# Optimization experiments

Hardware: AMD Instinct MI355X
Metric: run time of the kernel (lower is better)

The kernel has to match this reference:

```python
import jax, jax.numpy as jnp
import numpy as np
import math

NUM_HEADS = 16
ATTN_WIDTH = 256


def setup_inputs() -> dict:
    key = jax.random.key(0)
    ks = jax.random.split(key, 5)
    B, S, C, H = 2, 2048, 1024, 1024
    scale = 0.02
    return {
        "x": jax.random.normal(ks[0], (B, S, C), dtype=jnp.float32),
        "Wq": jax.random.normal(ks[1], (C, H), dtype=jnp.float32) * scale,
        "Wk": jax.random.normal(ks[2], (C, H), dtype=jnp.float32) * scale,
        "Wv": jax.random.normal(ks[3], (C, H), dtype=jnp.float32) * scale,
        "Wo": jax.random.normal(ks[4], (H, C), dtype=jnp.float32) * scale,
    }


def reference(x, Wq, Wk, Wv, Wo):
    B, S, C = x.shape
    H = NUM_HEADS
    dh = Wq.shape[1] // H  # head dim; Q.size(-1) in torch code

    def split_heads(t):
        # [B, S, H*dh] -> [B, H, S, dh]
        return t.reshape(B, S, H, dh).transpose(0, 2, 1, 3)

    q = split_heads(x @ Wq)
    k = split_heads(x @ Wk)
    v = split_heads(x @ Wv)

    scores = jnp.einsum("bhqd,bhkd->bhqk", q, k) / math.sqrt(dh)
    # exp-shift (first 'softmax-like' step, unnormalized)
    scores = jnp.exp(scores - jnp.max(scores, axis=-1, keepdims=True))
    # banded mask: tril(attn_width//2 - 1).triu(-(attn_width//2))
    i = jnp.arange(S)[:, None]
    j = jnp.arange(S)[None, :]
    d = j - i
    half = ATTN_WIDTH // 2
    mask = (d <= half - 1) & (d >= -half)
    scores = jnp.where(mask, scores, 0.0)
    # second softmax over the masked exp-scores (zeros contribute exp(0)=1)
    weights = jax.nn.softmax(scores, axis=-1)

    out = jnp.einsum("bhqk,bhkd->bhqd", weights, v)  # [B, H, S, dh]
    out = out.transpose(0, 2, 1, 3).reshape(B, S, H * dh)
    return out @ Wo
```

## Files before the change

### kernel.cpp

```cpp
#include <hip/hip_runtime.h>
#include <math.h>

typedef __bf16 bf16_t;
typedef bf16_t bf16x8 __attribute__((ext_vector_type(8)));
typedef bf16_t bf16x4 __attribute__((ext_vector_type(4)));
typedef float f32x4 __attribute__((ext_vector_type(4)));

constexpr int S_ = 2048;
constexpr float SCALE = 0.125f;

#define MFMA_B16(a, b, c) __builtin_amdgcn_mfma_f32_16x16x32_bf16(a, b, c, 0, 0, 0)

#define WAIT_VM0() __builtin_amdgcn_s_waitcnt(0x0F70)
#define WAIT_VM4() __builtin_amdgcn_s_waitcnt(0x0F74)
#define BARRIER()  __builtin_amdgcn_s_barrier()

typedef __attribute__((address_space(1))) const void* as1_cvp;
typedef __attribute__((address_space(3))) void* as3_vp;

__device__ __forceinline__ void gl2lds16(const void* g, void* l)
{
    __builtin_amdgcn_global_load_lds((as1_cvp)g, (as3_vp)l, 16, 0, 0);
}

#define SRC_SWZ8(lane) ((((lane) & 3) ^ (((lane) >> 3) & 3)) * 8)
#define RD_SWZ8(quad, l15) ((((quad) ^ (((l15) >> 1) & 3))) * 8)

__global__ __launch_bounds__(256) void prep(const float* __restrict__ x,
                                            const float* __restrict__ Wq,
                                            const float* __restrict__ Wk,
                                            const float* __restrict__ Wv,
                                            const float* __restrict__ Wo,
                                            bf16_t* __restrict__ xb,
                                            bf16_t* __restrict__ Wqt,
                                            bf16_t* __restrict__ Wkt,
                                            bf16_t* __restrict__ Wvt,
                                            bf16_t* __restrict__ Wot,
                                            float* __restrict__ vsp)
{
    __shared__ float T[64][65];
    const int blk = blockIdx.x;
    const int tid = threadIdx.x;
    if (blk < 1024) {
#pragma unroll
        for (int u = 0; u < 4; ++u) {
            const int g = blk * 1024 + u * 256 + tid;
            const float4 v = ((const float4*)x)[g];
            bf16x4 o;
            o[0] = (bf16_t)v.x; o[1] = (bf16_t)v.y;
            o[2] = (bf16_t)v.z; o[3] = (bf16_t)v.w;
            *(bf16x4*)&xb[(size_t)g * 4] = o;
        }
    } else if (blk < 2048) {
        const int rem = blk - 1024;
        const int wsel = rem >> 8, t = rem & 255;
        const float* src = (wsel == 0) ? Wq : (wsel == 1) ? Wk : (wsel == 2) ? Wv : Wo;
        bf16_t* dst = (wsel == 0) ? Wqt : (wsel == 1) ? Wkt : (wsel == 2) ? Wvt : Wot;
        const int k0 = (t >> 4) * 64, n0 = (t & 15) * 64;
        const int rr = tid >> 4, c4 = (tid & 15) * 4;
#pragma unroll
        for (int u = 0; u < 4; ++u) {
            const float4 v = *(const float4*)&src[(size_t)(k0 + u * 16 + rr) * 1024 + n0 + c4];
            T[u * 16 + rr][c4 + 0] = v.x; T[u * 16 + rr][c4 + 1] = v.y;
            T[u * 16 + rr][c4 + 2] = v.z; T[u * 16 + rr][c4 + 3] = v.w;
        }
        __syncthreads();
#pragma unroll
        for (int u = 0; u < 4; ++u) {
            bf16x4 o;
#pragma unroll
            for (int e = 0; e < 4; ++e) o[e] = (bf16_t)T[c4 + e][u * 16 + rr];
            *(bf16x4*)&dst[(size_t)(n0 + u * 16 + rr) * 1024 + k0 + c4] = o;
        }
    } else {
#pragma unroll
        for (int u = 0; u < 8; ++u) vsp[u * 256 + tid] = 0.f;
    }
}

template <int MODE>
__device__ __forceinline__ void mfma_gemm_body(const bf16_t* __restrict__ A,
                                               const bf16_t* __restrict__ Bt,
                                               void* __restrict__ dst,
                                               float* __restrict__ vsum_out,
                                               int m0, int n0)
{
    __shared__ bf16_t As[12288];
    __shared__ bf16_t Bs[12288];

    const int tid = threadIdx.x;
    const int lane = tid & 63, wid = tid >> 6;
    const int l15 = lane & 15, quad = lane >> 4;
    const int wm = (wid & 1) * 64, wn = (wid >> 1) * 64;

    const int srow = wid * 32 + (lane >> 2);
    const int scg8 = SRC_SWZ8(lane);
    const bf16_t* Ag0 = A  + (size_t)(m0 + srow) * 1024 + scg8;
    const bf16_t* Ag1 = A  + (size_t)(m0 + srow + 16) * 1024 + scg8;
    const bf16_t* Bg0 = Bt + (size_t)(n0 + srow) * 1024 + scg8;
    const bf16_t* Bg1 = Bt + (size_t)(n0 + srow + 16) * 1024 + scg8;

    const int rs = RD_SWZ8(quad, l15);

    f32x4 acc[4][4];
#pragma unroll
    for (int i = 0; i < 4; ++i)
#pragma unroll
        for (int j = 0; j < 4; ++j) acc[i][j] = (f32x4){0.f, 0.f, 0.f, 0.f};

#pragma unroll
    for (int p = 0; p < 2; ++p) {
        const int k0 = p * 32;
        gl2lds16(Ag0 + k0, As + p * 4096 + (wid * 2 + 0) * 512);
        gl2lds16(Ag1 + k0, As + p * 4096 + (wid * 2 + 1) * 512);
        gl2lds16(Bg0 + k0, Bs + p * 4096 + (wid * 2 + 0) * 512);
        gl2lds16(Bg1 + k0, Bs + p * 4096 + (wid * 2 + 1) * 512);
    }

#pragma unroll
    for (int it = 0; it < 32; ++it) {
        if (it < 30) WAIT_VM4(); else WAIT_VM0();
        BARRIER();
        if (it < 30) {
            const int k0 = (it + 2) * 32;
            const int sb = (it + 2) % 3;
            gl2lds16(Ag0 + k0, As + sb * 4096 + (wid * 2 + 0) * 512);
            gl2lds16(Ag1 + k0, As + sb * 4096 + (wid * 2 + 1) * 512);
            gl2lds16(Bg0 + k0, Bs + sb * 4096 + (wid * 2 + 0) * 512);
            gl2lds16(Bg1 + k0, Bs + sb * 4096 + (wid * 2 + 1) * 512);
        }
        const int cb = it % 3;
        bf16x8 af[4], bfr[4];
#pragma unroll
        for (int mt = 0; mt < 4; ++mt)
            af[mt] = *(const bf16x8*)&As[cb * 4096 + (wm + mt * 16 + l15) * 32 + rs];
#pragma unroll
        for (int nt = 0; nt < 4; ++nt)
            bfr[nt] = *(const bf16x8*)&Bs[cb * 4096 + (wn + nt * 16 + l15) * 32 + rs];
#pragma unroll
        for (int mt = 0; mt < 4; ++mt)
#pragma unroll
            for (int nt = 0; nt < 4; ++nt)
                acc[mt][nt] = MFMA_B16(bfr[nt], af[mt], acc[mt][nt]);
    }

#pragma unroll
    for (int mt = 0; mt < 4; ++mt) {
        const int m = m0 + wm + mt * 16 + l15;
#pragma unroll
        for (int nt = 0; nt < 4; ++nt) {
            const int nb = n0 + wn + nt * 16 + quad * 4;
            if (MODE == 0) {
                *(f32x4*)&((float*)dst)[(size_t)m * 1024 + nb] = acc[mt][nt];
            } else {
                const int bb = m >> 11, s = m & 2047;
                const int hh = nb >> 6, d = nb & 63;
                bf16x4 o;
#pragma unroll
                for (int u = 0; u < 4; ++u) o[u] = (bf16_t)acc[mt][nt][u];
                *(bf16x4*)&((bf16_t*)dst)[((size_t)(bb * 16 + hh) * 2048 + s) * 64 + d] = o;
            }
        }
    }

    if (MODE == 1 && vsum_out != nullptr) {
        const int bb = m0 >> 11;
#pragma unroll
        for (int nt = 0; nt < 4; ++nt) {
            f32x4 p = acc[0][nt];
#pragma unroll
            for (int mt = 1; mt < 4; ++mt) {
                p[0] += acc[mt][nt][0]; p[1] += acc[mt][nt][1];
                p[2] += acc[mt][nt][2]; p[3] += acc[mt][nt][3];
            }
#pragma unroll
            for (int st = 1; st < 16; st <<= 1) {
                p[0] += __shfl_xor(p[0], st);
                p[1] += __shfl_xor(p[1], st);
                p[2] += __shfl_xor(p[2], st);
                p[3] += __shfl_xor(p[3], st);
            }
            if (l15 == 0) {
                const int nI = n0 + wn + nt * 16 + quad * 4;
                float* vp = &vsum_out[(bb * 16 + (nI >> 6)) * 64 + (nI & 63)];
                atomicAdd(vp + 0, p[0]);
                atomicAdd(vp + 1, p[1]);
                atomicAdd(vp + 2, p[2]);
                atomicAdd(vp + 3, p[3]);
            }
        }
    }
}

__device__ __forceinline__ int remap_m(void) { return (blockIdx.x << 2) + (blockIdx.y >> 3); }
__device__ __forceinline__ int remap_n(void) { return blockIdx.y & 7; }

__global__ __launch_bounds__(256) void gemm_qkv_mfma(const bf16_t* __restrict__ xb,
                                                     const bf16_t* __restrict__ Wqt,
                                                     const bf16_t* __restrict__ Wkt,
                                                     const bf16_t* __restrict__ Wvt,
                                                     bf16_t* Qh, bf16_t* Kh, bf16_t* Vh,
                                                     float* vsp)
{
    const bf16_t* Bt = (blockIdx.z == 0) ? Wqt : (blockIdx.z == 1) ? Wkt : Wvt;
    bf16_t* dst = (blockIdx.z == 0) ? Qh : (blockIdx.z == 1) ? Kh : Vh;
    float* vs = (blockIdx.z == 2) ? vsp : nullptr;
    mfma_gemm_body<1>(xb, Bt, dst, vs, remap_m() * 128, remap_n() * 128);
}

__global__ __launch_bounds__(256) void gemm_out_mfma(const bf16_t* __restrict__ attn,
                                                     const bf16_t* __restrict__ Wot,
                                                     float* __restrict__ out)
{
    mfma_gemm_body<0>(attn, Wot, out, nullptr, remap_m() * 128, remap_n() * 128);
}

__global__ __launch_bounds__(256) void attn_k(const bf16_t* __restrict__ Qh,
                                              const bf16_t* __restrict__ Kh,
                                              const bf16_t* __restrict__ Vh,
                                              const float* __restrict__ vsp,
                                              bf16_t* __restrict__ attn)
{
    __shared__ bf16_t Qs[8192];
    __shared__ float mr_sh[128];
    __shared__ __align__(16) char uni[36352];

    bf16_t* KsA = (bf16_t*)uni;
    float*  msh = (float*)(uni + 32768);
    bf16_t* Ks2 = (bf16_t*)uni;
    bf16_t* Vt  = (bf16_t*)(uni + 8192);
    bf16_t* Ws  = (bf16_t*)(uni + 17408);
    float*  zsh = (float*)(uni + 35840);

    const int tid = threadIdx.x;
    const int lane = tid & 63, wid = tid >> 6;
    const int l15 = lane & 15, quad = lane >> 4;

    const int f = blockIdx.x;
    const int seq = f >> 3;
    const int bh = (f & 7) + 8 * (seq >> 4);
    const int i0 = (seq & 15) * 128;
    const int b = bh >> 4, h = bh & 15;
    const bf16_t* Qb = Qh + (size_t)bh * 131072;
    const bf16_t* Kb = Kh + (size_t)bh * 131072;
    const bf16_t* Vb = Vh + (size_t)bh * 131072;

    const int ssw = SRC_SWZ8(lane);
    const int rs  = RD_SWZ8(quad, l15);

    const int g    = wid * 4;
    const int srow = (lane >> 2);

#pragma unroll
    for (int c = 0; c < 4; ++c) {
        const int gg = g + c;
        const int half = gg >> 3;
        const int row = (gg & 7) * 16 + srow;
        gl2lds16(Qb + (size_t)(i0 + row) * 64 + half * 32 + ssw, Qs + gg * 512);
    }
#pragma unroll
    for (int c = 0; c < 4; ++c) {
        const int gg = g + c;
        const int half = gg >> 3;
        const int row = (gg & 7) * 16 + srow;
        gl2lds16(Kb + (size_t)row * 64 + half * 32 + ssw, KsA + gg * 512);
    }
    __syncthreads();

    bf16x8 af[8][2];
#pragma unroll
    for (int mt = 0; mt < 8; ++mt)
#pragma unroll
        for (int ks = 0; ks < 2; ++ks)
            af[mt][ks] = *(const bf16x8*)&Qs[ks * 4096 + (mt * 16 + l15) * 32 + rs];

    f32x4 vm[8];
#pragma unroll
    for (int mt = 0; mt < 8; ++mt)
        vm[mt] = (f32x4){-3.0e38f, -3.0e38f, -3.0e38f, -3.0e38f};

#pragma unroll 2
    for (int jc = 0; jc < 16; ++jc) {
        BARRIER();
        if (jc < 15) {
            const int sb = (jc + 1) & 1;
#pragma unroll
            for (int c = 0; c < 4; ++c) {
                const int gg = g + c;
                const int half = gg >> 3;
                const int row = (gg & 7) * 16 + srow;
                gl2lds16(Kb + (size_t)((jc + 1) * 128 + row) * 64 + half * 32 + ssw,
                         KsA + sb * 8192 + gg * 512);
            }
            WAIT_VM4();
        } else {
            WAIT_VM0();
        }
        BARRIER();

        const int cbuf = jc & 1;
#pragma unroll
        for (int ntl = 0; ntl < 2; ++ntl) {
            const int jt = wid * 2 + ntl;
            const bf16x8 b0 = *(const bf16x8*)&KsA[cbuf * 8192 + (jt * 16 + l15) * 32 + rs];
            const bf16x8 b1 = *(const bf16x8*)&KsA[cbuf * 8192 + 4096 + (jt * 16 + l15) * 32 + rs];
#pragma unroll
            for (int mt = 0; mt < 8; ++mt) {
                f32x4 t = (f32x4){0.f, 0.f, 0.f, 0.f};
                t = MFMA_B16(b0, af[mt][0], t);
                t = MFMA_B16(b1, af[mt][1], t);
                vm[mt][0] = fmaxf(vm[mt][0], t[0]);
                vm[mt][1] = fmaxf(vm[mt][1], t[1]);
                vm[mt][2] = fmaxf(vm[mt][2], t[2]);
                vm[mt][3] = fmaxf(vm[mt][3], t[3]);
            }
        }
    }

#pragma unroll
    for (int mt = 0; mt < 8; ++mt) {
        float v = fmaxf(fmaxf(vm[mt][0], vm[mt][1]), fmaxf(vm[mt][2], vm[mt][3]));
        v = fmaxf(v, __shfl_xor(v, 16));
        v = fmaxf(v, __shfl_xor(v, 32));
        if (quad == 0) msh[(wid * 8 + mt) * 16 + l15] = v;
    }
    __syncthreads();

    if (tid < 128) {
        const int mt = tid >> 4, il = tid & 15;
        const float v = fmaxf(fmaxf(msh[(0 * 8 + mt) * 16 + il], msh[(1 * 8 + mt) * 16 + il]),
                              fmaxf(msh[(2 * 8 + mt) * 16 + il], msh[(3 * 8 + mt) * 16 + il]));
        mr_sh[tid] = v * SCALE;
    }
    __syncthreads();

    bf16x8 aq[2][2];
#pragma unroll
    for (int t = 0; t < 2; ++t)
#pragma unroll
        for (int ks = 0; ks < 2; ++ks)
            aq[t][ks] = *(const bf16x8*)&Qs[ks * 4096 + ((wid * 2 + t) * 16 + l15) * 32 + rs];

    float mreg[2][4];
#pragma unroll
    for (int t = 0; t < 2; ++t)
#pragma unroll
        for (int r = 0; r < 4; ++r)
            mreg[t][r] = mr_sh[(wid * 2 + t) * 16 + quad * 4 + r];

    f32x4 vsd4[4];
#pragma unroll
    for (int dt = 0; dt < 4; ++dt)
        vsd4[dt] = *(const f32x4*)&vsp[bh * 64 + dt * 16 + quad * 4];

    f32x4 accO[2][4];
#pragma unroll
    for (int t = 0; t < 2; ++t)
#pragma unroll
        for (int dt = 0; dt < 4; ++dt) accO[t][dt] = (f32x4){0.f, 0.f, 0.f, 0.f};
    float zp[2][4] = {{0.f, 0.f, 0.f, 0.f}, {0.f, 0.f, 0.f, 0.f}};

    for (int cb2 = 0; cb2 < 6; ++cb2) {
        const int jb = i0 - 128 + cb2 * 64;
        if (jb < 0 || jb >= S_) continue;

        __syncthreads();
#pragma unroll
        for (int c = 0; c < 2; ++c) {
            const int gg = wid * 2 + c;
            const int half = gg >> 2;
            const int row = (gg & 3) * 16 + (lane >> 2);
            gl2lds16(Kb + (size_t)(jb + row) * 64 + half * 32 + ssw,
                     Ks2 + gg * 512);
        }
        {
            const bf16x8 v0 = *(const bf16x8*)&Vb[(size_t)(jb + lane) * 64 + wid * 16];
            const bf16x8 v1 = *(const bf16x8*)&Vb[(size_t)(jb + lane) * 64 + wid * 16 + 8];
#pragma unroll
            for (int e = 0; e < 8; ++e) {
                Vt[(wid * 16 + e) * 72 + lane] = v0[e];
                Vt[(wid * 16 + 8 + e) * 72 + lane] = v1[e];
            }
        }
        __syncthreads();

#pragma unroll
        for (int t = 0; t < 2; ++t) {
            const int mt = wid * 2 + t;
#pragma unroll
            for (int jt4 = 0; jt4 < 4; ++jt4) {
                const bf16x8 k0 = *(const bf16x8*)&Ks2[(jt4 * 16 + l15) * 32 + rs];
                const bf16x8 k1 = *(const bf16x8*)&Ks2[2048 + (jt4 * 16 + l15) * 32 + rs];
                f32x4 sc = (f32x4){0.f, 0.f, 0.f, 0.f};
                sc = MFMA_B16(aq[t][0], k0, sc);
                sc = MFMA_B16(aq[t][1], k1, sc);
#pragma unroll
                for (int r = 0; r < 4; ++r) {
                    const int ig = i0 + mt * 16 + quad * 4 + r;
                    const int jg = jb + jt4 * 16 + l15;
                    const int dd = jg - ig;
                    const bool ok = (dd >= -128) && (dd <= 127);
                    const float e1 = __expf(sc[r] * SCALE - mreg[t][r]);
                    const float wv = ok ? (__expf(e1) - 1.0f) : 0.0f;
                    const bf16_t wb = (bf16_t)wv;
                    zp[t][r] += (float)wb;
                    Ws[(mt * 16 + quad * 4 + r) * 72 + jt4 * 16 + l15] = wb;
                }
            }
        }
        __syncthreads();

#pragma unroll
        for (int ks = 0; ks < 2; ++ks) {
            bf16x8 bv[4];
#pragma unroll
            for (int dt = 0; dt < 4; ++dt)
                bv[dt] = *(const bf16x8*)&Vt[(dt * 16 + l15) * 72 + ks * 32 + quad * 8];
#pragma unroll
            for (int t = 0; t < 2; ++t) {
                const int mt = wid * 2 + t;
                const bf16x8 aw = *(const bf16x8*)&Ws[(mt * 16 + l15) * 72 + ks * 32 + quad * 8];
#pragma unroll
                for (int dt = 0; dt < 4; ++dt)
                    accO[t][dt] = MFMA_B16(bv[dt], aw, accO[t][dt]);
            }
        }
    }

#pragma unroll
    for (int t = 0; t < 2; ++t)
#pragma unroll
        for (int r = 0; r < 4; ++r) {
            float z = zp[t][r];
            z += __shfl_xor(z, 1);
            z += __shfl_xor(z, 2);
            z += __shfl_xor(z, 4);
            z += __shfl_xor(z, 8);
            if (l15 == 0) zsh[wid * 32 + t * 16 + quad * 4 + r] = z + (float)S_;
        }
    __syncthreads();

#pragma unroll
    for (int t = 0; t < 2; ++t) {
        const float rz = 1.0f / zsh[wid * 32 + t * 16 + l15];
        const int irow = i0 + (wid * 2 + t) * 16 + l15;
#pragma unroll
        for (int dt = 0; dt < 4; ++dt) {
            bf16x4 o;
#pragma unroll
            for (int r = 0; r < 4; ++r)
                o[r] = (bf16_t)((accO[t][dt][r] + vsd4[dt][r]) * rz);
            *(bf16x4*)&attn[(size_t)(b * S_ + irow) * 1024 + h * 64 + dt * 16 + quad * 4] = o;
        }
    }
}

extern "C" void kernel_launch(void* const* d_in, const int* in_sizes, int n_in,
                              void* d_out, int out_size, void* d_ws, size_t ws_size,
                              hipStream_t stream)
{
    const float* x  = (const float*)d_in[0];
    const float* Wq = (const float*)d_in[1];
    const float* Wk = (const float*)d_in[2];
    const float* Wv = (const float*)d_in[3];
    const float* Wo = (const float*)d_in[4];
    float* out = (float*)d_out;

    char* ws = (char*)d_ws;
    bf16_t* xb   = (bf16_t*)(ws + 0);
    bf16_t* Wqt  = (bf16_t*)(ws + 8388608);
    bf16_t* Wkt  = (bf16_t*)(ws + 10485760);
    bf16_t* Wvt  = (bf16_t*)(ws + 12582912);
    bf16_t* Wot  = (bf16_t*)(ws + 14680064);
    bf16_t* Qh   = (bf16_t*)(ws + 16777216);
    bf16_t* Kh   = (bf16_t*)(ws + 25165824);
    bf16_t* Vh   = (bf16_t*)(ws + 33554432);
    bf16_t* attn = (bf16_t*)(ws + 41943040);
    float*  vsp  = (float*)(ws + 50331648);

    prep<<<2049, 256, 0, stream>>>(x, Wq, Wk, Wv, Wo, xb, Wqt, Wkt, Wvt, Wot, vsp);
    gemm_qkv_mfma<<<dim3(8, 32, 3), 256, 0, stream>>>(xb, Wqt, Wkt, Wvt, Qh, Kh, Vh, vsp);
    attn_k<<<512, 256, 0, stream>>>(Qh, Kh, Vh, vsp, attn);
    gemm_out_mfma<<<dim3(8, 32), 256, 0, stream>>>(attn, Wot, out);
}
```

Measured before the change: 179.7 us.

## Emit V pre-transposed from QKV GEMM and deepen K-max prefetch pipeline

The QKV GEMM now computes V as Wv^T·x^T, so it writes V in [bh, d, s] layout and sums the V columns in the new orientation. The attention kernel can then load V tiles directly into LDS with async global-to-LDS copies and an XOR swizzle, instead of doing a register transpose through padded shared memory. The row-max pass switches from 128-row double-buffered K chunks to 64-row chunks with a 4-slot, 3-deep prefetch and one barrier per iteration. The risks are a less coalesced V store in the GEMM epilogue and more loop iterations in the max pass.

```diff
diff --git a/kernel.cpp b/kernel.cpp
--- a/kernel.cpp
+++ b/kernel.cpp
@@ -12,6 +12,7 @@
 #define MFMA_B16(a, b, c) __builtin_amdgcn_mfma_f32_16x16x32_bf16(a, b, c, 0, 0, 0)
 
 #define WAIT_VM0() __builtin_amdgcn_s_waitcnt(0x0F70)
+#define WAIT_VM2() __builtin_amdgcn_s_waitcnt(0x0F72)
 #define WAIT_VM4() __builtin_amdgcn_s_waitcnt(0x0F74)
 #define BARRIER()  __builtin_amdgcn_s_barrier()
 
@@ -79,15 +80,14 @@
 }
 
 template <int MODE>
-__device__ __forceinline__ void mfma_gemm_body(const bf16_t* __restrict__ A,
+__device__ __forceinline__ void mfma_gemm_body(bf16_t* __restrict__ As,
+                                               bf16_t* __restrict__ Bs,
+                                               const bf16_t* __restrict__ A,
                                                const bf16_t* __restrict__ Bt,
                                                void* __restrict__ dst,
                                                float* __restrict__ vsum_out,
                                                int m0, int n0)
 {
-    __shared__ bf16_t As[12288];
-    __shared__ bf16_t Bs[12288];
-
     const int tid = threadIdx.x;
     const int lane = tid & 63, wid = tid >> 6;
     const int l15 = lane & 15, quad = lane >> 4;
@@ -152,41 +152,37 @@
             const int nb = n0 + wn + nt * 16 + quad * 4;
             if (MODE == 0) {
                 *(f32x4*)&((float*)dst)[(size_t)m * 1024 + nb] = acc[mt][nt];
-            } else {
+            } else if (MODE == 1) {
                 const int bb = m >> 11, s = m & 2047;
                 const int hh = nb >> 6, d = nb & 63;
                 bf16x4 o;
 #pragma unroll
                 for (int u = 0; u < 4; ++u) o[u] = (bf16_t)acc[mt][nt][u];
                 *(bf16x4*)&((bf16_t*)dst)[((size_t)(bb * 16 + hh) * 2048 + s) * 64 + d] = o;
+            } else {
+                const int bb = n0 >> 11;
+                const int hh = m >> 6, dd = m & 63;
+                bf16x4 o;
+#pragma unroll
+                for (int u = 0; u < 4; ++u) o[u] = (bf16_t)acc[mt][nt][u];
+                *(bf16x4*)&((bf16_t*)dst)[((size_t)(bb * 16 + hh) * 64 + dd) * 2048 + (nb & 2047)] = o;
             }
         }
     }
 
-    if (MODE == 1 && vsum_out != nullptr) {
-        const int bb = m0 >> 11;
-#pragma unroll
-        for (int nt = 0; nt < 4; ++nt) {
-            f32x4 p = acc[0][nt];
-#pragma unroll
-            for (int mt = 1; mt < 4; ++mt) {
-                p[0] += acc[mt][nt][0]; p[1] += acc[mt][nt][1];
-                p[2] += acc[mt][nt][2]; p[3] += acc[mt][nt][3];
-            }
-#pragma unroll
-            for (int st = 1; st < 16; st <<= 1) {
-                p[0] += __shfl_xor(p[0], st);
-                p[1] += __shfl_xor(p[1], st);
-                p[2] += __shfl_xor(p[2], st);
-                p[3] += __shfl_xor(p[3], st);
-            }
-            if (l15 == 0) {
-                const int nI = n0 + wn + nt * 16 + quad * 4;
-                float* vp = &vsum_out[(bb * 16 + (nI >> 6)) * 64 + (nI & 63)];
-                atomicAdd(vp + 0, p[0]);
-                atomicAdd(vp + 1, p[1]);
-                atomicAdd(vp + 2, p[2]);
-                atomicAdd(vp + 3, p[3]);
+    if (MODE == 2 && vsum_out != nullptr) {
+        const int bb = n0 >> 11;
+#pragma unroll
+        for (int mt = 0; mt < 4; ++mt) {
+            float p = 0.f;
+#pragma unroll
+            for (int nt = 0; nt < 4; ++nt)
+                p += acc[mt][nt][0] + acc[mt][nt][1] + acc[mt][nt][2] + acc[mt][nt][3];
+            p += __shfl_xor(p, 16);
+            p += __shfl_xor(p, 32);
+            if (quad == 0) {
+                const int m = m0 + wm + mt * 16 + l15;
+                atomicAdd(&vsum_out[(bb * 16 + (m >> 6)) * 64 + (m & 63)], p);
             }
         }
     }
@@ -199,38 +195,45 @@
                                                      const bf16_t* __restrict__ Wqt,
                                                      const bf16_t* __restrict__ Wkt,
                                                      const bf16_t* __restrict__ Wvt,
-                                                     bf16_t* Qh, bf16_t* Kh, bf16_t* Vh,
+                                                     bf16_t* Qh, bf16_t* Kh, bf16_t* VhT,
                                                      float* vsp)
 {
-    const bf16_t* Bt = (blockIdx.z == 0) ? Wqt : (blockIdx.z == 1) ? Wkt : Wvt;
-    bf16_t* dst = (blockIdx.z == 0) ? Qh : (blockIdx.z == 1) ? Kh : Vh;
-    float* vs = (blockIdx.z == 2) ? vsp : nullptr;
-    mfma_gemm_body<1>(xb, Bt, dst, vs, remap_m() * 128, remap_n() * 128);
+    __shared__ bf16_t As[12288];
+    __shared__ bf16_t Bs[12288];
+    if (blockIdx.z == 2) {
+        mfma_gemm_body<2>(As, Bs, Wvt, xb, VhT, vsp, remap_n() * 128, remap_m() * 128);
+    } else {
+        const bf16_t* Bt = (blockIdx.z == 0) ? Wqt : Wkt;
+        bf16_t* dst = (blockIdx.z == 0) ? Qh : Kh;
+        mfma_gemm_body<1>(As, Bs, xb, Bt, dst, nullptr, remap_m() * 128, remap_n() * 128);
+    }
 }
 
 __global__ __launch_bounds__(256) void gemm_out_mfma(const bf16_t* __restrict__ attn,
                                                      const bf16_t* __restrict__ Wot,
                                                      float* __restrict__ out)
 {
-    mfma_gemm_body<0>(attn, Wot, out, nullptr, remap_m() * 128, remap_n() * 128);
+    __shared__ bf16_t As[12288];
+    __shared__ bf16_t Bs[12288];
+    mfma_gemm_body<0>(As, Bs, attn, Wot, out, nullptr, remap_m() * 128, remap_n() * 128);
 }
 
 __global__ __launch_bounds__(256) void attn_k(const bf16_t* __restrict__ Qh,
                                               const bf16_t* __restrict__ Kh,
-                                              const bf16_t* __restrict__ Vh,
+                                              const bf16_t* __restrict__ VhT,
                                               const float* __restrict__ vsp,
                                               bf16_t* __restrict__ attn)
 {
     __shared__ bf16_t Qs[8192];
     __shared__ float mr_sh[128];
-    __shared__ __align__(16) char uni[36352];
-
-    bf16_t* KsA = (bf16_t*)uni;
+    __shared__ __align__(16) char uni[35328];
+
+    bf16_t* KsB = (bf16_t*)uni;
     float*  msh = (float*)(uni + 32768);
     bf16_t* Ks2 = (bf16_t*)uni;
-    bf16_t* Vt  = (bf16_t*)(uni + 8192);
-    bf16_t* Ws  = (bf16_t*)(uni + 17408);
-    float*  zsh = (float*)(uni + 35840);
+    bf16_t* VtL = (bf16_t*)(uni + 8192);
+    bf16_t* Ws  = (bf16_t*)(uni + 16384);
+    float*  zsh = (float*)(uni + 34816);
 
     const int tid = threadIdx.x;
     const int lane = tid & 63, wid = tid >> 6;
@@ -241,30 +244,30 @@
     const int bh = (f & 7) + 8 * (seq >> 4);
     const int i0 = (seq & 15) * 128;
     const int b = bh >> 4, h = bh & 15;
-    const bf16_t* Qb = Qh + (size_t)bh * 131072;
-    const bf16_t* Kb = Kh + (size_t)bh * 131072;
-    const bf16_t* Vb = Vh + (size_t)bh * 131072;
+    const bf16_t* Qb  = Qh  + (size_t)bh * 131072;
+    const bf16_t* Kb  = Kh  + (size_t)bh * 131072;
+    const bf16_t* VbT = VhT + (size_t)bh * 131072;
 
     const int ssw = SRC_SWZ8(lane);
     const int rs  = RD_SWZ8(quad, l15);
 
-    const int g    = wid * 4;
-    const int srow = (lane >> 2);
-
 #pragma unroll
     for (int c = 0; c < 4; ++c) {
-        const int gg = g + c;
+        const int gg = wid * 4 + c;
         const int half = gg >> 3;
-        const int row = (gg & 7) * 16 + srow;
+        const int row = (gg & 7) * 16 + (lane >> 2);
         gl2lds16(Qb + (size_t)(i0 + row) * 64 + half * 32 + ssw, Qs + gg * 512);
     }
 #pragma unroll
-    for (int c = 0; c < 4; ++c) {
-        const int gg = g + c;
-        const int half = gg >> 3;
-        const int row = (gg & 7) * 16 + srow;
-        gl2lds16(Kb + (size_t)row * 64 + half * 32 + ssw, KsA + gg * 512);
-    }
+    for (int p = 0; p < 3; ++p)
+#pragma unroll
+        for (int c = 0; c < 2; ++c) {
+            const int gg = wid * 2 + c;
+            const int half = gg >> 2;
+            const int row = (gg & 3) * 16 + (lane >> 2);
+            gl2lds16(Kb + (size_t)(p * 64 + row) * 64 + half * 32 + ssw,
+                     KsB + p * 4096 + gg * 512);
+        }
     __syncthreads();
 
     bf16x8 af[8][2];
@@ -274,52 +277,42 @@
         for (int ks = 0; ks < 2; ++ks)
             af[mt][ks] = *(const bf16x8*)&Qs[ks * 4096 + (mt * 16 + l15) * 32 + rs];
 
-    f32x4 vm[8];
-#pragma unroll
-    for (int mt = 0; mt < 8; ++mt)
-        vm[mt] = (f32x4){-3.0e38f, -3.0e38f, -3.0e38f, -3.0e38f};
-
-#pragma unroll 2
-    for (int jc = 0; jc < 16; ++jc) {
+    float vm[8];
+#pragma unroll
+    for (int mt = 0; mt < 8; ++mt) vm[mt] = -3.0e38f;
+
+    for (int jc = 0; jc < 32; ++jc) {
+        if (jc < 30) WAIT_VM4();
+        else if (jc == 30) WAIT_VM2();
+        else WAIT_VM0();
         BARRIER();
-        if (jc < 15) {
-            const int sb = (jc + 1) & 1;
-#pragma unroll
-            for (int c = 0; c < 4; ++c) {
-                const int gg = g + c;
-                const int half = gg >> 3;
-                const int row = (gg & 7) * 16 + srow;
-                gl2lds16(Kb + (size_t)((jc + 1) * 128 + row) * 64 + half * 32 + ssw,
-                         KsA + sb * 8192 + gg * 512);
+        if (jc < 29) {
+            const int sb = (jc + 3) & 3;
+#pragma unroll
+            for (int c = 0; c < 2; ++c) {
+                const int gg = wid * 2 + c;
+                const int half = gg >> 2;
+                const int row = (gg & 3) * 16 + (lane >> 2);
+                gl2lds16(Kb + (size_t)((jc + 3) * 64 + row) * 64 + half * 32 + ssw,
+                         KsB + sb * 4096 + gg * 512);
             }
-            WAIT_VM4();
-        } else {
-            WAIT_VM0();
-        }
-        BARRIER();
-
-        const int cbuf = jc & 1;
-#pragma unroll
-        for (int ntl = 0; ntl < 2; ++ntl) {
-            const int jt = wid * 2 + ntl;
-            const bf16x8 b0 = *(const bf16x8*)&KsA[cbuf * 8192 + (jt * 16 + l15) * 32 + rs];
-            const bf16x8 b1 = *(const bf16x8*)&KsA[cbuf * 8192 + 4096 + (jt * 16 + l15) * 32 + rs];
-#pragma unroll
-            for (int mt = 0; mt < 8; ++mt) {
-                f32x4 t = (f32x4){0.f, 0.f, 0.f, 0.f};
-                t = MFMA_B16(b0, af[mt][0], t);
-                t = MFMA_B16(b1, af[mt][1], t);
-                vm[mt][0] = fmaxf(vm[mt][0], t[0]);
-                vm[mt][1] = fmaxf(vm[mt][1], t[1]);
-                vm[mt][2] = fmaxf(vm[mt][2], t[2]);
-                vm[mt][3] = fmaxf(vm[mt][3], t[3]);
-            }
+        }
+        const int cb = jc & 3;
+        const bf16x8 b0 = *(const bf16x8*)&KsB[cb * 4096 + (wid * 16 + l15) * 32 + rs];
+        const bf16x8 b1 = *(const bf16x8*)&KsB[cb * 4096 + 2048 + (wid * 16 + l15) * 32 + rs];
+#pragma unroll
+        for (int mt = 0; mt < 8; ++mt) {
+            f32x4 t = (f32x4){0.f, 0.f, 0.f, 0.f};
+            t = MFMA_B16(b0, af[mt][0], t);
+            t = MFMA_B16(b1, af[mt][1], t);
+            const float u = fmaxf(fmaxf(t[0], t[1]), t[2]);
+            vm[mt] = fmaxf(fmaxf(u, t[3]), vm[mt]);
         }
     }
 
 #pragma unroll
     for (int mt = 0; mt < 8; ++mt) {
-        float v = fmaxf(fmaxf(vm[mt][0], vm[mt][1]), fmaxf(vm[mt][2], vm[mt][3]));
+        float v = vm[mt];
         v = fmaxf(v, __shfl_xor(v, 16));
         v = fmaxf(v, __shfl_xor(v, 32));
         if (quad == 0) msh[(wid * 8 + mt) * 16 + l15] = v;
@@ -370,17 +363,14 @@
             const int gg = wid * 2 + c;
             const int half = gg >> 2;
             const int row = (gg & 3) * 16 + (lane >> 2);
-            gl2lds16(Kb + (size_t)(jb + row) * 64 + half * 32 + ssw,
-                     Ks2 + gg * 512);
-        }
-        {
-            const bf16x8 v0 = *(const bf16x8*)&Vb[(size_t)(jb + lane) * 64 + wid * 16];
-            const bf16x8 v1 = *(const bf16x8*)&Vb[(size_t)(jb + lane) * 64 + wid * 16 + 8];
-#pragma unroll
-            for (int e = 0; e < 8; ++e) {
-                Vt[(wid * 16 + e) * 72 + lane] = v0[e];
-                Vt[(wid * 16 + 8 + e) * 72 + lane] = v1[e];
-            }
+            gl2lds16(Kb + (size_t)(jb + row) * 64 + half * 32 + ssw, Ks2 + gg * 512);
+        }
+#pragma unroll
+        for (int c = 0; c < 2; ++c) {
+            const int gg = wid * 2 + c;
+            const int d = gg * 8 + (lane >> 3);
+            const int jl = (lane & 7) ^ ((lane >> 3) & 7);
+            gl2lds16(VbT + (size_t)d * 2048 + jb + jl * 8, VtL + gg * 512);
         }
         __syncthreads();
 
@@ -415,7 +405,8 @@
             bf16x8 bv[4];
 #pragma unroll
             for (int dt = 0; dt < 4; ++dt)
-                bv[dt] = *(const bf16x8*)&Vt[(dt * 16 + l15) * 72 + ks * 32 + quad * 8];
+                bv[dt] = *(const bf16x8*)&VtL[(dt * 16 + l15) * 64 +
+                                              (((ks * 4 + quad) ^ (l15 & 7)) * 8)];
 #pragma unroll
             for (int t = 0; t < 2; ++t) {
                 const int mt = wid * 2 + t;
@@ -474,12 +465,12 @@
     bf16_t* Wot  = (bf16_t*)(ws + 14680064);
     bf16_t* Qh   = (bf16_t*)(ws + 16777216);
     bf16_t* Kh   = (bf16_t*)(ws + 25165824);
-    bf16_t* Vh   = (bf16_t*)(ws + 33554432);
+    bf16_t* VhT  = (bf16_t*)(ws + 33554432);
     bf16_t* attn = (bf16_t*)(ws + 41943040);
     float*  vsp  = (float*)(ws + 50331648);
 
     prep<<<2049, 256, 0, stream>>>(x, Wq, Wk, Wv, Wo, xb, Wqt, Wkt, Wvt, Wot, vsp);
-    gemm_qkv_mfma<<<dim3(8, 32, 3), 256, 0, stream>>>(xb, Wqt, Wkt, Wvt, Qh, Kh, Vh, vsp);
-    attn_k<<<512, 256, 0, stream>>>(Qh, Kh, Vh, vsp, attn);
+    gemm_qkv_mfma<<<dim3(8, 32, 3), 256, 0, stream>>>(xb, Wqt, Wkt, Wvt, Qh, Kh, VhT, vsp);
+    attn_k<<<512, 256, 0, stream>>>(Qh, Kh, VhT, vsp, attn);
     gemm_out_mfma<<<dim3(8, 32), 256, 0, stream>>>(attn, Wot, out);
 }
```

Result: no change. 179.1 us (-0.3%).
